# Kernel tuning notes

Measured on AMD Instinct MI355X. Metric: run time of the kernel, lower is better.

The kernel has to match this reference:

```python
import jax, jax.numpy as jnp
import numpy as np

N, E, G = 50000, 800000, 512
DIN, H, DOUT, L = 128, 256, 128, 5
H4 = 4 * H


def _ffnn(h, W1, b1, W2, b2):
    # Linear -> exact GELU (torch default) -> Linear
    return jax.nn.gelu(h @ W1 + b1, approximate=False) @ W2 + b2


def _mean_pool(h, batch):
    s = jax.ops.segment_sum(h, batch, num_segments=G)
    c = jax.ops.segment_sum(jnp.ones((h.shape[0], 1), h.dtype), batch, num_segments=G)
    return s / jnp.maximum(c, 1.0)


def setup_inputs() -> dict:
    key = jax.random.key(0)
    ks = iter(jax.random.split(key, 64))
    w = lambda *s: jax.random.normal(next(ks), s, jnp.float32) * 0.02
    z = lambda *s: jnp.zeros(s, jnp.float32)
    inp = {
        'x': jax.random.normal(next(ks), (N, DIN), jnp.float32),
        'edge_index': jax.random.randint(next(ks), (2, E), 0, N, jnp.int32),
        'batch': jnp.sort(jax.random.randint(next(ks), (N,), 0, G, jnp.int32)),
        'pre_W1': w(DIN, H), 'pre_b1': z(H), 'pre_W2': w(H, H), 'pre_b2': z(H),
        'gin_W1': w(L, H, H), 'gin_b1': z(L, H), 'gin_W2': w(L, H, H), 'gin_b2': z(L, H),
        'ffn_W1': w(L, H, H), 'ffn_b1': z(L, H), 'ffn_W2': w(L, H, H), 'ffn_b2': z(L, H),
        'upd_W1': w(L, H, H), 'upd_b1': z(L, H), 'upd_W2': w(L, H, H4), 'upd_b2': z(L, H4),
        'prop_W1': w(L, H4, H), 'prop_b1': z(L, H), 'prop_W2': w(L, H, H), 'prop_b2': z(L, H),
        'bn_gamma': jnp.ones((L, H), jnp.float32), 'bn_beta': z(L, H),
        'vn': jax.random.normal(next(ks), (1, H4), jnp.float32),
        'post_W1': w(H, H), 'post_b1': z(H), 'post_W2': w(H, DOUT), 'post_b2': z(DOUT),
    }
    return inp


def reference(x, edge_index, batch,
              pre_W1, pre_b1, pre_W2, pre_b2,
              gin_W1, gin_b1, gin_W2, gin_b2,
              ffn_W1, ffn_b1, ffn_W2, ffn_b2,
              upd_W1, upd_b1, upd_W2, upd_b2,
              prop_W1, prop_b1, prop_W2, prop_b2,
              bn_gamma, bn_beta, vn,
              post_W1, post_b1, post_W2, post_b2):
    src, dst = edge_index[0], edge_index[1]
    h = _ffnn(x, pre_W1, pre_b1, pre_W2, pre_b2)
    for i in range(L):
        # virtual node update and propagation
        v = vn + _ffnn(_mean_pool(h, batch), upd_W1[i], upd_b1[i], upd_W2[i], upd_b2[i])  # [G, 4H]
        outvn = _ffnn(v, prop_W1[i], prop_b1[i], prop_W2[i], prop_b2[i])  # [G, H]
        # GINConv (eps=0): nn((1+eps)*h + sum_{j->i} h_j), residual
        agg = jax.ops.segment_sum(h[src], dst, num_segments=N)
        h = _ffnn(h + agg, gin_W1[i], gin_b1[i], gin_W2[i], gin_b2[i]) + h
        # BatchNorm1d (batch statistics, biased var)
        mu = jnp.mean(h, axis=0)
        var = jnp.mean((h - mu) ** 2, axis=0)
        h = (h - mu) * jax.lax.rsqrt(var + 1e-5) * bn_gamma[i] + bn_beta[i]
        # broadcast VN to nodes, FFNN with residual (dropout = identity in eval)
        h = _ffnn(outvn[batch] + h, ffn_W1[i], ffn_b1[i], ffn_W2[i], ffn_b2[i]) + h
    out = _ffnn(_mean_pool(h, batch), post_W1, post_b1, post_W2, post_b2)
    return out
```

## Files before the change

kernel.cpp:

```cpp
#include <hip/hip_runtime.h>
#include <hip/hip_bf16.h>
#include <math.h>

#define NN 50000
#define NNP 50048
#define NE 800000
#define NG 512
#define DIN 128
#define HD 256
#define DOUT 128
#define NL 5
#define H4 1024

typedef _Float16 f16x8 __attribute__((ext_vector_type(8)));
typedef _Float16 f16x4 __attribute__((ext_vector_type(4)));
typedef float f32x4 __attribute__((ext_vector_type(4)));

__device__ __forceinline__ float gelu_exact(float x) {
    return 0.5f * x * (1.0f + erff(x * 0.70710678118654752f));
}

__device__ __forceinline__ void gl_lds16(const _Float16* g, _Float16* l) {
    __builtin_amdgcn_global_load_lds(
        (const __attribute__((address_space(1))) unsigned int*)g,
        (__attribute__((address_space(3))) unsigned int*)l, 16, 0, 0);
}

__global__ void k_hist(const int* __restrict__ idx, int* __restrict__ cnt, int n) {
    int i = blockIdx.x * blockDim.x + threadIdx.x;
    if (i < n) atomicAdd(&cnt[idx[i]], 1);
}

__global__ void k_scan_small(const int* __restrict__ in, int* __restrict__ out, int n) {
    __shared__ int buf[1024];
    int t = threadIdx.x;
    int v = (t < n) ? in[t] : 0;
    buf[t] = v;
    __syncthreads();
    for (int off = 1; off < 1024; off <<= 1) {
        int x = (t >= off) ? buf[t - off] : 0;
        __syncthreads();
        buf[t] += x;
        __syncthreads();
    }
    if (t < n) out[t] = buf[t] - v;
    if (t == 1023) out[n] = buf[1023];
}

__global__ void k_scan_part(const int* __restrict__ in, int* __restrict__ bsum, int n) {
    __shared__ int buf[256];
    int i = blockIdx.x * 256 + threadIdx.x;
    buf[threadIdx.x] = (i < n) ? in[i] : 0;
    __syncthreads();
    for (int off = 128; off > 0; off >>= 1) {
        if (threadIdx.x < off) buf[threadIdx.x] += buf[threadIdx.x + off];
        __syncthreads();
    }
    if (threadIdx.x == 0) bsum[blockIdx.x] = buf[0];
}

__global__ void k_scan_mid(const int* __restrict__ bsum, int* __restrict__ bexcl, int nb,
                           int* __restrict__ out, int n) {
    __shared__ int buf[1024];
    int t = threadIdx.x;
    int v = (t < nb) ? bsum[t] : 0;
    buf[t] = v;
    __syncthreads();
    for (int off = 1; off < 1024; off <<= 1) {
        int x = (t >= off) ? buf[t - off] : 0;
        __syncthreads();
        buf[t] += x;
        __syncthreads();
    }
    if (t < nb) bexcl[t] = buf[t] - v;
    if (t == 1023) out[n] = buf[1023];
}

__global__ void k_scan_out(const int* __restrict__ in, const int* __restrict__ bexcl,
                           int* __restrict__ out, int n) {
    __shared__ int buf[256];
    int i = blockIdx.x * 256 + threadIdx.x;
    int t = threadIdx.x;
    int v = (i < n) ? in[i] : 0;
    buf[t] = v;
    __syncthreads();
    for (int off = 1; off < 256; off <<= 1) {
        int x = (t >= off) ? buf[t - off] : 0;
        __syncthreads();
        buf[t] += x;
        __syncthreads();
    }
    if (i < n) out[i] = bexcl[blockIdx.x] + buf[t] - v;
}

__global__ void k_fill_csr(const int* __restrict__ src, const int* __restrict__ dst,
                           const int* __restrict__ eoff, int* __restrict__ cursor,
                           int* __restrict__ csr, int n) {
    int e = blockIdx.x * blockDim.x + threadIdx.x;
    if (e < n) {
        int d = dst[e];
        int p = atomicAdd(&cursor[d], 1);
        csr[eoff[d] + p] = src[e];
    }
}

__global__ void k_cvt16(const float* __restrict__ in, _Float16* __restrict__ out, int n4) {
    int i = blockIdx.x * blockDim.x + threadIdx.x;
    if (i < n4) {
        float4 v = *(const float4*)&in[i * 4];
        f16x4 o = { (_Float16)v.x, (_Float16)v.y, (_Float16)v.z, (_Float16)v.w };
        *(f16x4*)&out[i * 4] = o;
    }
}

#define NWTJOBS 44
struct WtJobs {
    const float* src[NWTJOBS];
    _Float16* dst[NWTJOBS];
    short K32[NWTJOBS];
    short N32[NWTJOBS];
    short pre[NWTJOBS + 1];
};
__global__ void k_wtb(WtJobs j) {
    int bid = blockIdx.x;
    int lo = 0;
    while (j.pre[lo + 1] <= bid) ++lo;
    int tl = bid - j.pre[lo];
    int nx = j.N32[lo];
    int n0 = (tl % nx) * 32, k0 = (tl / nx) * 32;
    int K = j.K32[lo] * 32, N = nx * 32;
    const float* W = j.src[lo];
    _Float16* Wt = j.dst[lo];
    __shared__ float tile[32][33];
    for (int i = threadIdx.y; i < 32; i += 8)
        tile[i][threadIdx.x] = W[(size_t)(k0 + i) * N + n0 + threadIdx.x];
    __syncthreads();
    for (int i = threadIdx.y; i < 32; i += 8)
        Wt[(size_t)(n0 + i) * K + k0 + threadIdx.x] = (_Float16)tile[threadIdx.x][i];
}

__global__ void k_pool16(const _Float16* __restrict__ h16, const int* __restrict__ goff,
                         _Float16* __restrict__ pool) {
    int g = blockIdx.x;
    int c = threadIdx.x;
    int s = goff[g], e = goff[g + 1];
    float acc = 0.f;
    for (int r = s; r < e; ++r) acc += (float)h16[(size_t)r * HD + c];
    int cnt = e - s;
    pool[g * HD + c] = (_Float16)(acc / (float)(cnt > 0 ? cnt : 1));
}

__global__ __launch_bounds__(256) void k_agg16(const _Float16* __restrict__ h16,
                                               const int* __restrict__ eoff,
                                               const int* __restrict__ csr,
                                               _Float16* __restrict__ out) {
    int node = blockIdx.x * 4 + (threadIdx.x >> 6);
    int lane = threadIdx.x & 63;
    int half = lane >> 5, l = lane & 31;
    f16x8 mine = *(const f16x8*)&h16[(size_t)node * HD + l * 8];
    float acc[8];
#pragma unroll
    for (int q = 0; q < 8; ++q) acc[q] = half ? 0.f : (float)mine[q];
    int s = eoff[node], e = eoff[node + 1];
    for (int base = s; base < e; base += 64) {
        int myi = base + lane;
        int vidx = (myi < e) ? csr[myi] : 0;
        int cnt = min(64, e - base);
        int jj = 0;
        for (; jj + 7 < cnt; jj += 8) {
            int s0 = __shfl(vidx, jj + half);
            int s1 = __shfl(vidx, jj + 2 + half);
            int s2 = __shfl(vidx, jj + 4 + half);
            int s3 = __shfl(vidx, jj + 6 + half);
            f16x8 v0 = *(const f16x8*)&h16[(size_t)s0 * HD + l * 8];
            f16x8 v1 = *(const f16x8*)&h16[(size_t)s1 * HD + l * 8];
            f16x8 v2 = *(const f16x8*)&h16[(size_t)s2 * HD + l * 8];
            f16x8 v3 = *(const f16x8*)&h16[(size_t)s3 * HD + l * 8];
#pragma unroll
            for (int q = 0; q < 8; ++q)
                acc[q] += ((float)v0[q] + (float)v1[q]) + ((float)v2[q] + (float)v3[q]);
        }
        for (; jj + 3 < cnt; jj += 4) {
            int s0 = __shfl(vidx, jj + half);
            int s1 = __shfl(vidx, jj + 2 + half);
            f16x8 v0 = *(const f16x8*)&h16[(size_t)s0 * HD + l * 8];
            f16x8 v1 = *(const f16x8*)&h16[(size_t)s1 * HD + l * 8];
#pragma unroll
            for (int q = 0; q < 8; ++q) acc[q] += (float)v0[q] + (float)v1[q];
        }
        for (; jj < cnt; jj += 2) {
            int i0 = jj + half;
            int s0 = __shfl(vidx, i0);
            if (i0 < cnt) {
                f16x8 v0 = *(const f16x8*)&h16[(size_t)s0 * HD + l * 8];
#pragma unroll
                for (int q = 0; q < 8; ++q) acc[q] += (float)v0[q];
            }
        }
    }
#pragma unroll
    for (int q = 0; q < 8; ++q) acc[q] += __shfl_xor(acc[q], 32);
    if (!half) {
        f16x8 o;
#pragma unroll
        for (int q = 0; q < 8; ++q) o[q] = (_Float16)acc[q];
        *(f16x8*)&out[(size_t)node * HD + l * 8] = o;
    }
}

__global__ void k_bn_final(float* __restrict__ stat,
                           const float* __restrict__ gamma, const float* __restrict__ beta,
                           float* __restrict__ scale, float* __restrict__ shift) {
    int c = threadIdx.x;
    float mu = stat[c] * (1.0f / NN);
    float var = stat[HD + c] * (1.0f / NN) - mu * mu;
    float rs = rsqrtf(var + 1e-5f);
    float sc = rs * gamma[c];
    scale[c] = sc;
    shift[c] = beta[c] - mu * sc;
    stat[c] = 0.f;
    stat[HD + c] = 0.f;
}

template <bool ABN1, bool RES2, bool RESBN2, bool STATS2, int K1>
__global__ __launch_bounds__(512) void k_b2b(const _Float16* __restrict__ A16,
                                             const _Float16* __restrict__ G16,
                                             const _Float16* __restrict__ W1t,
                                             const float* __restrict__ b1,
                                             const _Float16* __restrict__ W2t,
                                             const float* __restrict__ b2,
                                             const _Float16* __restrict__ R16,
                                             const float* __restrict__ bnsc,
                                             const float* __restrict__ bnsh,
                                             const float* __restrict__ ovn,
                                             const int* __restrict__ batchv,
                                             float* __restrict__ stat,
                                             _Float16* __restrict__ C16,
                                             int M) {
    __shared__ _Float16 AC[32][64][8];
    constexpr int NT1 = K1 >> 5;
    const int t = threadIdx.x;
    const int w = t >> 6, lane = t & 63;
    const int m0 = blockIdx.x * 64;
    const int kb = lane >> 4, fr = lane & 15, rr = lane >> 4;

    if constexpr (ABN1) {
        for (int c = t; c < K1 * 8; c += 512) {
            int kblk = c >> 6, row = c & 63;
            int b0 = batchv[min(m0 + row, M - 1)];
            const int c0 = kblk * 8;
            f16x8 g = *(const f16x8*)&G16[(size_t)(m0 + row) * HD + c0];
            f16x8 r0;
#pragma unroll
            for (int q = 0; q < 8; ++q)
                r0[q] = (_Float16)((float)g[q] * bnsc[c0 + q] + bnsh[c0 + q] +
                                   ovn[(size_t)b0 * HD + c0 + q]);
            *(f16x8*)&AC[kblk][row][0] = r0;
        }
    } else {
        for (int c = t; c < K1 * 8; c += 512) {
            int kblk = c >> 6, row = c & 63;
            gl_lds16(A16 + (size_t)(m0 + row) * K1 + kblk * 8, &AC[kblk][row][0]);
        }
    }
    __syncthreads();

    f32x4 acc1[4][2];
#pragma unroll
    for (int mi = 0; mi < 4; ++mi)
#pragma unroll
        for (int ni = 0; ni < 2; ++ni) acc1[mi][ni] = (f32x4){0.f, 0.f, 0.f, 0.f};

    {
        f16x8 bf[3][2];
        auto loadB = [&](int s, f16x8* dst) {
#pragma unroll
            for (int ni = 0; ni < 2; ++ni)
                dst[ni] = *(const f16x8*)&W1t[(size_t)(w * 32 + ni * 16 + fr) * K1 + (s << 5) + kb * 8];
        };
        loadB(0, bf[0]);
        if (NT1 > 1) loadB(1, bf[1]);
#pragma unroll
        for (int s = 0; s < NT1; ++s) {
            if (s + 2 < NT1) loadB(s + 2, bf[(s + 2) % 3]);
            f16x8 af[4];
#pragma unroll
            for (int mi = 0; mi < 4; ++mi)
                af[mi] = *(const f16x8*)&AC[(s << 2) + kb][mi * 16 + fr][0];
#pragma unroll
            for (int mi = 0; mi < 4; ++mi)
#pragma unroll
                for (int ni = 0; ni < 2; ++ni)
                    acc1[mi][ni] = __builtin_amdgcn_mfma_f32_16x16x32_f16(af[mi], bf[s % 3][ni], acc1[mi][ni], 0, 0, 0);
        }
    }

    __syncthreads();
#pragma unroll
    for (int mi = 0; mi < 4; ++mi) {
#pragma unroll
        for (int reg = 0; reg < 4; ++reg) {
            int ml = mi * 16 + rr * 4 + reg;
#pragma unroll
            for (int ni = 0; ni < 2; ++ni) {
                int n = w * 32 + ni * 16 + fr;
                float v = gelu_exact(acc1[mi][ni][reg] + b1[n]);
                AC[n >> 3][ml][n & 7] = (_Float16)v;
            }
        }
    }
    __syncthreads();

    f32x4 acc2[4][2];
#pragma unroll
    for (int mi = 0; mi < 4; ++mi)
#pragma unroll
        for (int ni = 0; ni < 2; ++ni) acc2[mi][ni] = (f32x4){0.f, 0.f, 0.f, 0.f};

    {
        f16x8 bf[3][2];
        auto loadB = [&](int s, f16x8* dst) {
#pragma unroll
            for (int ni = 0; ni < 2; ++ni)
                dst[ni] = *(const f16x8*)&W2t[(size_t)(w * 32 + ni * 16 + fr) * HD + (s << 5) + kb * 8];
        };
        loadB(0, bf[0]);
        loadB(1, bf[1]);
#pragma unroll
        for (int s = 0; s < 8; ++s) {
            if (s + 2 < 8) loadB(s + 2, bf[(s + 2) % 3]);
            f16x8 af[4];
#pragma unroll
            for (int mi = 0; mi < 4; ++mi)
                af[mi] = *(const f16x8*)&AC[s * 4 + kb][mi * 16 + fr][0];
#pragma unroll
            for (int mi = 0; mi < 4; ++mi)
#pragma unroll
                for (int ni = 0; ni < 2; ++ni)
                    acc2[mi][ni] = __builtin_amdgcn_mfma_f32_16x16x32_f16(af[mi], bf[s % 3][ni], acc2[mi][ni], 0, 0, 0);
        }
    }

    float cs[2] = {0.f, 0.f}, cq[2] = {0.f, 0.f};
#pragma unroll
    for (int mi = 0; mi < 4; ++mi) {
#pragma unroll
        for (int reg = 0; reg < 4; ++reg) {
            int m = m0 + mi * 16 + rr * 4 + reg;
            if (m < M) {
#pragma unroll
                for (int ni = 0; ni < 2; ++ni) {
                    int n = w * 32 + ni * 16 + fr;
                    float v = acc2[mi][ni][reg] + b2[n];
                    if (RES2) v += (float)R16[(size_t)m * HD + n];
                    if (RESBN2) v += (float)R16[(size_t)m * HD + n] * bnsc[n] + bnsh[n];
                    _Float16 vh = (_Float16)v;
                    C16[(size_t)m * HD + n] = vh;
                    if (STATS2) { float vr = (float)vh; cs[ni] += vr; cq[ni] += vr * vr; }
                }
            }
        }
    }
    if constexpr (STATS2) {
#pragma unroll
        for (int ni = 0; ni < 2; ++ni) {
            cs[ni] += __shfl_xor(cs[ni], 16); cs[ni] += __shfl_xor(cs[ni], 32);
            cq[ni] += __shfl_xor(cq[ni], 16); cq[ni] += __shfl_xor(cq[ni], 32);
        }
        if (lane < 16) {
#pragma unroll
            for (int ni = 0; ni < 2; ++ni) {
                int n = w * 32 + ni * 16 + lane;
                atomicAdd(&stat[n], cs[ni]);
                atomicAdd(&stat[HD + n], cq[ni]);
            }
        }
    }
}

template <bool GELU, bool BIAS2, bool O32, bool O16>
__global__ __launch_bounds__(256) void k_mgemm(const _Float16* __restrict__ A,
                                               const _Float16* __restrict__ Wt,
                                               const float* __restrict__ bias,
                                               const float* __restrict__ bias2,
                                               float* __restrict__ C32,
                                               _Float16* __restrict__ C16,
                                               int M, int N, int K) {
    __shared__ _Float16 As[2][4][64][8];
    __shared__ _Float16 Bs[2][4][128][8];
    const int t = threadIdx.x;
    const int w = t >> 6, lane = t & 63;
    const int m0 = blockIdx.y * 64, n0 = blockIdx.x * 128;
    const int kb = lane >> 4, fr = lane & 15;

    f32x4 acc[4][2];
#pragma unroll
    for (int mi = 0; mi < 4; ++mi)
#pragma unroll
        for (int ni = 0; ni < 2; ++ni) acc[mi][ni] = (f32x4){0.f, 0.f, 0.f, 0.f};

    const _Float16* gA0 = A + (size_t)(m0 + lane) * K + w * 8;
    const _Float16* gB0 = Wt + (size_t)(n0 + lane) * K + w * 8;
    const _Float16* gB1 = Wt + (size_t)(n0 + 64 + lane) * K + w * 8;

    auto stage = [&](int buf, int k0) {
        gl_lds16(gB0 + k0, &Bs[buf][w][0][0]);
        gl_lds16(gB1 + k0, &Bs[buf][w][64][0]);
        gl_lds16(gA0 + k0, &As[buf][w][0][0]);
    };

    const int nt = K >> 5;
    stage(0, 0);
    __syncthreads();
    for (int tt = 0; tt < nt; ++tt) {
        const int cur = tt & 1;
        if (tt + 1 < nt) stage(cur ^ 1, (tt + 1) << 5);
        f16x8 af[4], bf[2];
#pragma unroll
        for (int mi = 0; mi < 4; ++mi)
            af[mi] = *(const f16x8*)&As[cur][kb][mi * 16 + fr][0];
#pragma unroll
        for (int ni = 0; ni < 2; ++ni)
            bf[ni] = *(const f16x8*)&Bs[cur][kb][w * 32 + ni * 16 + fr][0];
#pragma unroll
        for (int mi = 0; mi < 4; ++mi)
#pragma unroll
            for (int ni = 0; ni < 2; ++ni)
                acc[mi][ni] = __builtin_amdgcn_mfma_f32_16x16x32_f16(af[mi], bf[ni], acc[mi][ni], 0, 0, 0);
        __syncthreads();
    }

    const int rr = lane >> 4;
#pragma unroll
    for (int mi = 0; mi < 4; ++mi) {
#pragma unroll
        for (int reg = 0; reg < 4; ++reg) {
            int m = m0 + mi * 16 + rr * 4 + reg;
            if (m < M) {
#pragma unroll
                for (int ni = 0; ni < 2; ++ni) {
                    int n = n0 + w * 32 + ni * 16 + fr;
                    float v = acc[mi][ni][reg] + bias[n];
                    if (BIAS2) v += bias2[n];
                    if (GELU) v = gelu_exact(v);
                    if (O32) C32[(size_t)m * N + n] = v;
                    if (O16) C16[(size_t)m * N + n] = (_Float16)v;
                }
            }
        }
    }
}

static inline void mg_gelu(hipStream_t st, const _Float16* A, const _Float16* Wt,
                           const float* bias, _Float16* C16, int M, int N, int K) {
    dim3 g(N / 128, (M + 63) / 64), b(256);
    k_mgemm<true, false, false, true><<<g, b, 0, st>>>(A, Wt, bias, nullptr, nullptr, C16, M, N, K);
}
static inline void mg_bias2_16(hipStream_t st, const _Float16* A, const _Float16* Wt,
                               const float* bias, const float* bias2, _Float16* C16,
                               int M, int N, int K) {
    dim3 g(N / 128, (M + 63) / 64), b(256);
    k_mgemm<false, true, false, true><<<g, b, 0, st>>>(A, Wt, bias, bias2, nullptr, C16, M, N, K);
}
static inline void mg_f32only(hipStream_t st, const _Float16* A, const _Float16* Wt,
                              const float* bias, float* C32, int M, int N, int K) {
    dim3 g(N / 128, (M + 63) / 64), b(256);
    k_mgemm<false, false, true, false><<<g, b, 0, st>>>(A, Wt, bias, nullptr, C32, nullptr, M, N, K);
}

extern "C" void kernel_launch(void* const* d_in, const int* in_sizes, int n_in,
                              void* d_out, int out_size, void* d_ws, size_t ws_size,
                              hipStream_t stream) {
    const float* x       = (const float*)d_in[0];
    const int*   ei      = (const int*)d_in[1];
    const int*   batch   = (const int*)d_in[2];
    const float* pre_W1  = (const float*)d_in[3];
    const float* pre_b1  = (const float*)d_in[4];
    const float* pre_W2  = (const float*)d_in[5];
    const float* pre_b2  = (const float*)d_in[6];
    const float* gin_W1  = (const float*)d_in[7];
    const float* gin_b1  = (const float*)d_in[8];
    const float* gin_W2  = (const float*)d_in[9];
    const float* gin_b2  = (const float*)d_in[10];
    const float* ffn_W1  = (const float*)d_in[11];
    const float* ffn_b1  = (const float*)d_in[12];
    const float* ffn_W2  = (const float*)d_in[13];
    const float* ffn_b2  = (const float*)d_in[14];
    const float* upd_W1  = (const float*)d_in[15];
    const float* upd_b1  = (const float*)d_in[16];
    const float* upd_W2  = (const float*)d_in[17];
    const float* upd_b2  = (const float*)d_in[18];
    const float* prop_W1 = (const float*)d_in[19];
    const float* prop_b1 = (const float*)d_in[20];
    const float* prop_W2 = (const float*)d_in[21];
    const float* prop_b2 = (const float*)d_in[22];
    const float* bn_gamma= (const float*)d_in[23];
    const float* bn_beta = (const float*)d_in[24];
    const float* vn      = (const float*)d_in[25];
    const float* post_W1 = (const float*)d_in[26];
    const float* post_b1 = (const float*)d_in[27];
    const float* post_W2 = (const float*)d_in[28];
    const float* post_b2 = (const float*)d_in[29];
    float* out = (float*)d_out;

    const int* e_src = ei;
    const int* e_dst = ei + NE;

    char* p = (char*)d_ws;
    auto alloc = [&](size_t bytes) -> char* {
        char* r = p;
        p += (bytes + 255) & ~(size_t)255;
        return r;
    };
    _Float16* h16    = (_Float16*)alloc((size_t)NNP * HD * 2);
    _Float16* g16    = (_Float16*)alloc((size_t)NNP * HD * 2);
    _Float16* t16a   = (_Float16*)alloc((size_t)NNP * HD * 2);
    _Float16* pool16 = (_Float16*)alloc((size_t)NG * HD * 2);
    _Float16* u16    = (_Float16*)alloc((size_t)NG * HD * 2);
    _Float16* vb16   = (_Float16*)alloc((size_t)NG * H4 * 2);
    _Float16* p16    = (_Float16*)alloc((size_t)NG * HD * 2);
    float*    outvn32= (float*)alloc((size_t)NG * HD * 4);
    float*    bnstat = (float*)alloc(2 * HD * 4);
    float*    bnscale= (float*)alloc(HD * 4);
    float*    bnshift= (float*)alloc(HD * 4);
    _Float16* preW1t = (_Float16*)alloc((size_t)HD * DIN * 2);
    _Float16* preW2t = (_Float16*)alloc((size_t)HD * HD * 2);
    _Float16* ginW1t = (_Float16*)alloc((size_t)NL * HD * HD * 2);
    _Float16* ginW2t = (_Float16*)alloc((size_t)NL * HD * HD * 2);
    _Float16* ffnW1t = (_Float16*)alloc((size_t)NL * HD * HD * 2);
    _Float16* ffnW2t = (_Float16*)alloc((size_t)NL * HD * HD * 2);
    _Float16* updW1t = (_Float16*)alloc((size_t)NL * HD * HD * 2);
    _Float16* updW2t = (_Float16*)alloc((size_t)NL * HD * H4 * 2);
    _Float16* propW1t= (_Float16*)alloc((size_t)NL * H4 * HD * 2);
    _Float16* propW2t= (_Float16*)alloc((size_t)NL * HD * HD * 2);
    _Float16* postW1t= (_Float16*)alloc((size_t)HD * HD * 2);
    _Float16* postW2t= (_Float16*)alloc((size_t)DOUT * HD * 2);
    int* gcount = (int*)alloc(NG * 4);
    int* goff   = (int*)alloc((NG + 1) * 4);
    int* deg    = (int*)alloc(NN * 4);
    int* eoff   = (int*)alloc((NN + 1) * 4);
    int* cursor = (int*)alloc(NN * 4);
    int* csr    = (int*)alloc((size_t)NE * 4);
    int* bsum   = (int*)alloc(1024 * 4);
    int* bexcl  = (int*)alloc(1024 * 4);
    _Float16* x16 = t16a;

    {
        size_t span = (size_t)((char*)(cursor + NN) - (char*)gcount);
        hipMemsetAsync(gcount, 0, span, stream);
        hipMemsetAsync(bnstat, 0, 2 * HD * 4, stream);
    }
    hipLaunchKernelGGL(k_hist, dim3((NN + 255) / 256), dim3(256), 0, stream, batch, gcount, NN);
    hipLaunchKernelGGL(k_hist, dim3((NE + 255) / 256), dim3(256), 0, stream, e_dst, deg, NE);
    hipLaunchKernelGGL(k_scan_small, dim3(1), dim3(1024), 0, stream, gcount, goff, NG);
    {
        int nbN = (NN + 255) / 256;
        hipLaunchKernelGGL(k_scan_part, dim3(nbN), dim3(256), 0, stream, deg, bsum, NN);
        hipLaunchKernelGGL(k_scan_mid, dim3(1), dim3(1024), 0, stream, bsum, bexcl, nbN, eoff, NN);
        hipLaunchKernelGGL(k_scan_out, dim3(nbN), dim3(256), 0, stream, deg, bexcl, eoff, NN);
    }
    hipLaunchKernelGGL(k_fill_csr, dim3((NE + 255) / 256), dim3(256), 0, stream, e_src, e_dst, eoff, cursor, csr, NE);

    {
        WtJobs j;
        int idx = 0, tiles = 0;
        auto add = [&](const float* s, _Float16* d, int K, int N) {
            j.src[idx] = s; j.dst[idx] = d;
            j.K32[idx] = (short)(K / 32); j.N32[idx] = (short)(N / 32);
            j.pre[idx] = (short)tiles;
            tiles += (K / 32) * (N / 32);
            ++idx;
        };
        add(pre_W1, preW1t, DIN, HD);
        add(pre_W2, preW2t, HD, HD);
        add(post_W1, postW1t, HD, HD);
        add(post_W2, postW2t, HD, DOUT);
        for (int i = 0; i < NL; ++i) {
            add(gin_W1 + (size_t)i * HD * HD, ginW1t + (size_t)i * HD * HD, HD, HD);
            add(gin_W2 + (size_t)i * HD * HD, ginW2t + (size_t)i * HD * HD, HD, HD);
            add(ffn_W1 + (size_t)i * HD * HD, ffnW1t + (size_t)i * HD * HD, HD, HD);
            add(ffn_W2 + (size_t)i * HD * HD, ffnW2t + (size_t)i * HD * HD, HD, HD);
            add(upd_W1 + (size_t)i * HD * HD, updW1t + (size_t)i * HD * HD, HD, HD);
            add(upd_W2 + (size_t)i * HD * H4, updW2t + (size_t)i * HD * H4, HD, H4);
            add(prop_W1 + (size_t)i * H4 * HD, propW1t + (size_t)i * H4 * HD, H4, HD);
            add(prop_W2 + (size_t)i * HD * HD, propW2t + (size_t)i * HD * HD, HD, HD);
        }
        j.pre[idx] = (short)tiles;
        hipLaunchKernelGGL(k_wtb, dim3(tiles), dim3(32, 8), 0, stream, j);
    }

    int n4 = NN * DIN / 4;
    hipLaunchKernelGGL(k_cvt16, dim3((n4 + 255) / 256), dim3(256), 0, stream, x, x16, n4);

    const int nb2b = NNP / 64;

    hipLaunchKernelGGL((k_b2b<false, false, false, false, DIN>), dim3(nb2b), dim3(512), 0, stream,
                       x16, nullptr, preW1t, pre_b1, preW2t, pre_b2,
                       nullptr, nullptr, nullptr, nullptr, nullptr, nullptr,
                       h16, NN);

    for (int i = 0; i < NL; ++i) {
        const _Float16* uW1 = updW1t + (size_t)i * HD * HD;
        const _Float16* uW2 = updW2t + (size_t)i * HD * H4;
        const _Float16* pW1 = propW1t + (size_t)i * H4 * HD;
        const _Float16* pW2 = propW2t + (size_t)i * HD * HD;

        hipLaunchKernelGGL(k_pool16, dim3(NG), dim3(HD), 0, stream, h16, goff, pool16);
        mg_gelu(stream, pool16, uW1, upd_b1 + (size_t)i * HD, u16, NG, HD, HD);
        mg_bias2_16(stream, u16, uW2, upd_b2 + (size_t)i * H4, vn, vb16, NG, H4, HD);
        mg_gelu(stream, vb16, pW1, prop_b1 + (size_t)i * HD, p16, NG, HD, H4);
        mg_f32only(stream, p16, pW2, prop_b2 + (size_t)i * HD, outvn32, NG, HD, HD);

        hipLaunchKernelGGL(k_agg16, dim3(NN / 4), dim3(256), 0, stream, h16, eoff, csr, t16a);
        hipLaunchKernelGGL((k_b2b<false, true, false, true, HD>), dim3(nb2b), dim3(512), 0, stream,
                           t16a, nullptr,
                           ginW1t + (size_t)i * HD * HD, gin_b1 + (size_t)i * HD,
                           ginW2t + (size_t)i * HD * HD, gin_b2 + (size_t)i * HD,
                           h16, nullptr, nullptr, nullptr, nullptr, bnstat,
                           g16, NN);

        hipLaunchKernelGGL(k_bn_final, dim3(1), dim3(HD), 0, stream, bnstat,
                           bn_gamma + (size_t)i * HD, bn_beta + (size_t)i * HD, bnscale, bnshift);

        hipLaunchKernelGGL((k_b2b<true, false, true, false, HD>), dim3(nb2b), dim3(512), 0, stream,
                           nullptr, g16,
                           ffnW1t + (size_t)i * HD * HD, ffn_b1 + (size_t)i * HD,
                           ffnW2t + (size_t)i * HD * HD, ffn_b2 + (size_t)i * HD,
                           g16, bnscale, bnshift, outvn32, batch, nullptr,
                           h16, NN);
    }

    hipLaunchKernelGGL(k_pool16, dim3(NG), dim3(HD), 0, stream, h16, goff, pool16);
    mg_gelu(stream, pool16, postW1t, post_b1, u16, NG, HD, HD);
    mg_f32only(stream, u16, postW2t, post_b2, out, NG, DOUT, HD);
}
```

Before: 1.639 ms.

## Approximate GELU erf, unroll pooling loop, and slice BN stat atomics

Replaces erff in GELU with the Abramowitz-Stegun polynomial using a fast reciprocal and exp, which makes GELU cheaper to evaluate in the fused GEMM epilogues. Unrolls the per-graph mean-pool loop into four independent accumulators so more loads are in flight. Spreads the BatchNorm statistic atomics across eight slices indexed by block, which the finalize kernel sums and clears, to reduce contention on the same addresses. The erf approximation has an error of roughly 1e-7 absolute, which sits near fp16 precision, so accuracy risk is small.

Measured after the change: 1.397 ms. -14.8%, faster.

```diff
diff --git a/kernel.cpp b/kernel.cpp
--- a/kernel.cpp
+++ b/kernel.cpp
@@ -11,13 +11,20 @@
 #define DOUT 128
 #define NL 5
 #define H4 1024
+#define NSL 8
 
 typedef _Float16 f16x8 __attribute__((ext_vector_type(8)));
 typedef _Float16 f16x4 __attribute__((ext_vector_type(4)));
 typedef float f32x4 __attribute__((ext_vector_type(4)));
 
 __device__ __forceinline__ float gelu_exact(float x) {
-    return 0.5f * x * (1.0f + erff(x * 0.70710678118654752f));
+    float ax = fabsf(x) * 0.70710678118654752f;
+    float t = __builtin_amdgcn_rcpf(1.0f + 0.3275911f * ax);
+    float poly = t * (0.254829592f + t * (-0.284496736f + t * (1.421413741f +
+                 t * (-1.453152027f + t * 1.061405429f))));
+    float erfv = 1.0f - poly * __expf(-ax * ax);
+    erfv = copysignf(erfv, x);
+    return 0.5f * x * (1.0f + erfv);
 }
 
 __device__ __forceinline__ void gl_lds16(const _Float16* g, _Float16* l) {
@@ -144,8 +151,16 @@
     int g = blockIdx.x;
     int c = threadIdx.x;
     int s = goff[g], e = goff[g + 1];
-    float acc = 0.f;
-    for (int r = s; r < e; ++r) acc += (float)h16[(size_t)r * HD + c];
+    float a0 = 0.f, a1 = 0.f, a2 = 0.f, a3 = 0.f;
+    int r = s;
+    for (; r + 3 < e; r += 4) {
+        a0 += (float)h16[(size_t)r * HD + c];
+        a1 += (float)h16[(size_t)(r + 1) * HD + c];
+        a2 += (float)h16[(size_t)(r + 2) * HD + c];
+        a3 += (float)h16[(size_t)(r + 3) * HD + c];
+    }
+    for (; r < e; ++r) a0 += (float)h16[(size_t)r * HD + c];
+    float acc = (a0 + a1) + (a2 + a3);
     int cnt = e - s;
     pool[g * HD + c] = (_Float16)(acc / (float)(cnt > 0 ? cnt : 1));
 }
@@ -212,14 +227,20 @@
                            const float* __restrict__ gamma, const float* __restrict__ beta,
                            float* __restrict__ scale, float* __restrict__ shift) {
     int c = threadIdx.x;
-    float mu = stat[c] * (1.0f / NN);
-    float var = stat[HD + c] * (1.0f / NN) - mu * mu;
+    float s = 0.f, q = 0.f;
+#pragma unroll
+    for (int k = 0; k < NSL; ++k) {
+        s += stat[k * 2 * HD + c];
+        q += stat[k * 2 * HD + HD + c];
+        stat[k * 2 * HD + c] = 0.f;
+        stat[k * 2 * HD + HD + c] = 0.f;
+    }
+    float mu = s * (1.0f / NN);
+    float var = q * (1.0f / NN) - mu * mu;
     float rs = rsqrtf(var + 1e-5f);
     float sc = rs * gamma[c];
     scale[c] = sc;
     shift[c] = beta[c] - mu * sc;
-    stat[c] = 0.f;
-    stat[HD + c] = 0.f;
 }
 
 template <bool ABN1, bool RES2, bool RESBN2, bool STATS2, int K1>
@@ -362,6 +383,7 @@
         }
     }
     if constexpr (STATS2) {
+        float* slice = stat + (size_t)(blockIdx.x & (NSL - 1)) * 2 * HD;
 #pragma unroll
         for (int ni = 0; ni < 2; ++ni) {
             cs[ni] += __shfl_xor(cs[ni], 16); cs[ni] += __shfl_xor(cs[ni], 32);
@@ -371,8 +393,8 @@
 #pragma unroll
             for (int ni = 0; ni < 2; ++ni) {
                 int n = w * 32 + ni * 16 + lane;
-                atomicAdd(&stat[n], cs[ni]);
-                atomicAdd(&stat[HD + n], cq[ni]);
+                atomicAdd(&slice[n], cs[ni]);
+                atomicAdd(&slice[HD + n], cq[ni]);
             }
         }
     }
@@ -520,7 +542,7 @@
     _Float16* vb16   = (_Float16*)alloc((size_t)NG * H4 * 2);
     _Float16* p16    = (_Float16*)alloc((size_t)NG * HD * 2);
     float*    outvn32= (float*)alloc((size_t)NG * HD * 4);
-    float*    bnstat = (float*)alloc(2 * HD * 4);
+    float*    bnstat = (float*)alloc((size_t)NSL * 2 * HD * 4);
     float*    bnscale= (float*)alloc(HD * 4);
     float*    bnshift= (float*)alloc(HD * 4);
     _Float16* preW1t = (_Float16*)alloc((size_t)HD * DIN * 2);
@@ -548,7 +570,7 @@
     {
         size_t span = (size_t)((char*)(cursor + NN) - (char*)gcount);
         hipMemsetAsync(gcount, 0, span, stream);
-        hipMemsetAsync(bnstat, 0, 2 * HD * 4, stream);
+        hipMemsetAsync(bnstat, 0, (size_t)NSL * 2 * HD * 4, stream);
     }
     hipLaunchKernelGGL(k_hist, dim3((NN + 255) / 256), dim3(256), 0, stream, batch, gcount, NN);
     hipLaunchKernelGGL(k_hist, dim3((NE + 255) / 256), dim3(256), 0, stream, e_dst, deg, NE);
```
